# Kernel optimization log

Measured on AMD Instinct MI355X. Metric: run time of the kernel, lower is better.

## Reference

```python
import jax, jax.numpy as jnp
from jax import lax
import numpy as np

B, N, J, NI, D = 2, 2048, 24, 9, 3
CD, HID = 16, 128
SOFT_BLEND = 20.0
MAX_STEPS, CVG = 50, 1e-5
INIT_BONES = np.array([0, 1, 2, 4, 5, 16, 17, 18, 19])


def _mlp(params, x):
    h = x
    for W, b in params[:-1]:
        h = jax.nn.softplus(h @ W + b)
    W, b = params[-1]
    return h @ W + b


def _broyden(g, x0, J_inv0):
    # x0: [P,3,1], J_inv0: [P,3,3]; fixed MAX_STEPS iterations, track best iterate
    gx = g(x0)
    err0 = jnp.linalg.norm(gx, axis=(1, 2))
    state = (x0, gx, J_inv0, -(J_inv0 @ gx), x0, err0)

    def body(i, st):
        x, gx, Jinv, upd, bx, berr = st
        dx = upd
        x = x + dx
        gx_new = g(x)
        dgx = gx_new - gx
        vT = jnp.swapaxes(dx, -2, -1) @ Jinv            # [P,1,3]
        a = dx - Jinv @ dgx                              # [P,3,1]
        b = vT @ dgx + 1e-6                              # [P,1,1]
        Jinv = Jinv + (a / b) @ vT                       # rank-1 Broyden update
        upd = -(Jinv @ gx_new)
        err = jnp.linalg.norm(gx_new, axis=(1, 2))
        better = err < berr
        bx = jnp.where(better[:, None, None], x, bx)
        berr = jnp.where(better, err, berr)
        return (x, gx_new, Jinv, upd, bx, berr)

    st = lax.fori_loop(0, MAX_STEPS, body, state)
    return st[4], st[5] < CVG


def setup_inputs():
    key = jax.random.key(0)
    ks = jax.random.split(key, 24)
    xd = 0.5 * jax.random.normal(ks[0], (B, N, D), jnp.float32)
    cond_latent = jax.random.normal(ks[1], (B, CD), jnp.float32)
    # near-identity invertible bone transforms
    R = jnp.eye(3, dtype=jnp.float32) + 0.1 * jax.random.normal(ks[2], (B, J, 3, 3), jnp.float32)
    t = 0.1 * jax.random.normal(ks[3], (B, J, 3), jnp.float32)
    tfs = jnp.zeros((B, J, 4, 4), jnp.float32)
    tfs = tfs.at[..., :3, :3].set(R).at[..., :3, 3].set(t).at[..., 3, 3].set(1.0)

    def w(k, fi, fo):
        return jax.random.normal(k, (fi, fo), jnp.float32) / np.sqrt(fi)

    din = D + CD
    inp = dict(xd=xd, cond_latent=cond_latent, tfs=tfs)
    dims_lbs = [(din, HID), (HID, HID), (HID, HID), (HID, J)]
    dims_disp = [(din, HID), (HID, HID), (HID, HID), (HID, D)]
    for i, (fi, fo) in enumerate(dims_lbs):
        inp[f"lbs_w{i}"] = w(ks[4 + i], fi, fo)
        inp[f"lbs_b{i}"] = jnp.zeros((fo,), jnp.float32)
    for i, (fi, fo) in enumerate(dims_disp):
        inp[f"disp_w{i}"] = w(ks[10 + i], fi, fo)
        inp[f"disp_b{i}"] = jnp.zeros((fo,), jnp.float32)
    return inp


def _forward(xd, cond_latent, tfs, lbs, disp):
    P = B * N
    xd_f = xd.reshape(P, D)
    cond_f = jnp.broadcast_to(cond_latent[:, None], (B, N, CD)).reshape(P, CD)
    tfs_f = jnp.broadcast_to(tfs[:, None], (B, N, J, 4, 4)).reshape(P, J, 4, 4)

    # __init: inverse-skin xd with one-hot weights at each init bone -> [P, NI, 3]
    xd_h = jnp.concatenate([xd_f, jnp.ones((P, 1), xd.dtype)], -1)
    xc_init = jnp.einsum('pnij,pj->pni', jnp.linalg.inv(tfs_f[:, INIT_BONES]), xd_h)[..., :3]

    PI = P * NI
    cond_e = jnp.repeat(cond_f, NI, axis=0)       # [PI, CD]
    tfs_e = jnp.repeat(tfs_f, NI, axis=0)         # [PI, J, 4, 4]
    xd_tgt = jnp.repeat(xd_f, NI, axis=0)         # [PI, 3]
    x0 = xc_init.reshape(PI, D)

    def fwd_skin(xc, lbs_p, cond_p, tfs_p):
        w = jax.nn.softmax(SOFT_BLEND * _mlp(lbs_p, jnp.concatenate([xc, cond_p], -1)), -1)
        xh = jnp.concatenate([xc, jnp.ones_like(xc[:, :1])], -1)
        return jnp.einsum('pn,pnij,pj->pi', w, tfs_p, xh)[:, :3]

    def fwd_skin_pt(x, c, t, lbs_p):
        w = jax.nn.softmax(SOFT_BLEND * _mlp(lbs_p, jnp.concatenate([x, c])))
        xh = jnp.concatenate([x, jnp.ones((1,), x.dtype)])
        return jnp.einsum('n,nij,j->i', w, t, xh)[:3]

    def gradient(xc, lbs_p, cond_p, tfs_p):
        # per-point 3x3 Jacobian of forward skinning wrt canonical point
        f = lambda x, c, t: fwd_skin_pt(x, c, t, lbs_p)
        return jax.vmap(jax.jacfwd(f), in_axes=(0, 0, 0))(xc, cond_p, tfs_p)

    # stop-gradient copies for the no-grad broyden search (torch.no_grad block)
    sg = lax.stop_gradient
    lbs_sg = [(sg(W), sg(b)) for W, b in lbs]
    cond_sg, tfs_sg, xdt_sg = sg(cond_e), sg(tfs_e), sg(xd_tgt)

    J_inv0 = jnp.linalg.inv(gradient(sg(x0), lbs_sg, cond_sg, tfs_sg))

    def g_ng(x):  # x: [PI,3,1]
        return (fwd_skin(x[..., 0], lbs_sg, cond_sg, tfs_sg) - xdt_sg)[..., None]

    x_opt, valid = _broyden(g_ng, sg(x0)[..., None], J_inv0)
    xc_opt = sg(x_opt[..., 0])

    # implicit-differentiation correction (eval_mode=False path)
    xd_opt = fwd_skin(xc_opt, lbs, cond_e, tfs_e)
    grad_inv = jnp.linalg.inv(gradient(xc_opt, lbs, cond_e, tfs_e))
    corr = jnp.einsum('pij,pj->pi', -sg(grad_inv), xd_opt - sg(xd_opt))
    xc = xc_opt + corr

    # __query_cano: beta displacement network
    xc = xc + _mlp(disp, jnp.concatenate([xc, cond_e], -1))
    return xc.reshape(B, N, NI, D), valid.reshape(B, N, NI)


def reference(xd, cond_latent, tfs, lbs_w0, lbs_b0, lbs_w1, lbs_b1, lbs_w2, lbs_b2, lbs_w3, lbs_b3, disp_w0, disp_b0, disp_w1, disp_b1, disp_w2, disp_b2, disp_w3, disp_b3):
    lbs = [(lbs_w0, lbs_b0), (lbs_w1, lbs_b1), (lbs_w2, lbs_b2), (lbs_w3, lbs_b3)]
    disp = [(disp_w0, disp_b0), (disp_w1, disp_b1), (disp_w2, disp_b2), (disp_w3, disp_b3)]
    return _forward(xd, cond_latent, tfs, lbs, disp)
```

## Files before the change

### kernel.cpp

```cpp
#include <hip/hip_runtime.h>
#include <hip/hip_bf16.h>
#include <math.h>

#define NB 2
#define NN 2048
#define NJ 24
#define NIB 9
#define NCD 16
#define NHID 128
#define NP (NB * NN)
#define NPI (NP * NIB)
#define NBSTRIDE (NN * NIB)
#define SBLEND 20.0f
#define CVG_EPS 1e-5f
#define MAX_STEPS 50

#define HSTR 129
#define INSTRD 21
#define LSTR 25

static __device__ __forceinline__ float softplusf(float x) {
    return fmaxf(x, 0.0f) + log1pf(expf(-fabsf(x)));
}
static __device__ __forceinline__ float sigmoidf(float x) {
    return 1.0f / (1.0f + expf(-x));
}
static __device__ __forceinline__ int bone_of(int ib) {
    return (ib < 3) ? ib : ((ib < 5) ? ib + 1 : ib + 11);
}

template <int K>
static __device__ __forceinline__ void mv_acc32(const float* __restrict__ Wp, const float* inrow,
                                                int jb, float* acc) {
#pragma unroll 4
    for (int k = 0; k < K; k++) {
        float h = inrow[k];
        const float* wk = Wp + k * NHID + jb;
#pragma unroll
        for (int jj = 0; jj < 32; jj++) acc[jj] = fmaf(h, wk[jj], acc[jj]);
    }
}

template <int K, int LDIN>
static __device__ __forceinline__ void val_layer(const float* __restrict__ Wp,
                                                 const float* __restrict__ bp,
                                                 const float* inbase, float (*Hs)[HSTR], int r,
                                                 int jb, bool prebar) {
    float acc[32];
#pragma unroll
    for (int jj = 0; jj < 32; jj++) acc[jj] = bp[jb + jj];
    mv_acc32<K>(Wp, inbase + r * LDIN, jb, acc);
    if (prebar) __syncthreads();
#pragma unroll
    for (int jj = 0; jj < 32; jj++) Hs[r][jb + jj] = softplusf(acc[jj]);
    __syncthreads();
}

template <int K, int LDIN>
static __device__ __forceinline__ void jac_layer(const float* __restrict__ Wp,
                                                 const float* __restrict__ bp,
                                                 const float* inbase, float (*Hs)[HSTR], int r,
                                                 int jb, bool prebar) {
    const bool isval = (r < 16);
    const int p = r & 15;
    float acc[32];
#pragma unroll
    for (int jj = 0; jj < 32; jj++) acc[jj] = isval ? bp[jb + jj] : 0.0f;
    mv_acc32<K>(Wp, inbase + r * LDIN, jb, acc);
    if (prebar) __syncthreads();
#pragma unroll
    for (int jj = 0; jj < 32; jj++) Hs[r][jb + jj] = acc[jj];
    __syncthreads();
    float zv[32];
    if (!isval) {
#pragma unroll
        for (int jj = 0; jj < 32; jj++) zv[jj] = Hs[p][jb + jj];
    }
    __syncthreads();
    if (isval) {
#pragma unroll
        for (int jj = 0; jj < 32; jj++) Hs[r][jb + jj] = softplusf(acc[jj]);
    } else {
#pragma unroll
        for (int jj = 0; jj < 32; jj++) Hs[r][jb + jj] = sigmoidf(zv[jj]) * acc[jj];
    }
    __syncthreads();
}

template <int NC, int LDW, bool JAC>
static __device__ __forceinline__ void logit_layer(const float* __restrict__ Wp,
                                                   const float* __restrict__ bp,
                                                   const float* inbase, float (*Lgs)[LSTR], int r,
                                                   int wid) {
    const int jb = wid * NC;
    const bool isval = (!JAC) || (r < 16);
    float acc[NC];
#pragma unroll
    for (int jj = 0; jj < NC; jj++) acc[jj] = isval ? bp[jb + jj] : 0.0f;
#pragma unroll 4
    for (int k = 0; k < NHID; k++) {
        float h = inbase[r * HSTR + k];
        const float* wk = Wp + k * LDW + jb;
#pragma unroll
        for (int jj = 0; jj < NC; jj++) acc[jj] = fmaf(h, wk[jj], acc[jj]);
    }
#pragma unroll
    for (int jj = 0; jj < NC; jj++) Lgs[r][jb + jj] = acc[jj];
    __syncthreads();
}

__global__ __launch_bounds__(256) void kernel_fused(
    const float* __restrict__ xd, const float* __restrict__ cond, const float* __restrict__ tfs,
    const float* __restrict__ lw0, const float* __restrict__ lb0,
    const float* __restrict__ lw1, const float* __restrict__ lb1,
    const float* __restrict__ lw2, const float* __restrict__ lb2,
    const float* __restrict__ lw3, const float* __restrict__ lb3,
    const float* __restrict__ dw0, const float* __restrict__ db0,
    const float* __restrict__ dw1, const float* __restrict__ db1,
    const float* __restrict__ dw2, const float* __restrict__ db2,
    const float* __restrict__ dw3, const float* __restrict__ db3,
    float* __restrict__ out) {
    __shared__ float sIN[64][INSTRD];
    __shared__ float sH[64][HSTR];
    __shared__ float sLg[64][LSTR];
    __shared__ float sTm[NJ * 12];
    __shared__ int sFlag;

    const int tid = threadIdx.x;
    const int r = tid & 63;
    const int wid = __builtin_amdgcn_readfirstlane(tid >> 6);
    const int jb = wid * 32;
    const int pi0 = blockIdx.x * 64;
    const int b = pi0 / NBSTRIDE;
    const int pi = pi0 + r;

    for (int t = tid; t < NJ * 12; t += 256) {
        int j = t / 12, rc = t % 12;
        sTm[t] = tfs[(size_t)(b * NJ + j) * 16 + rc];
    }
    if (tid >= 16 && tid < 64) {
        const int d = (tid >> 4) - 1;
#pragma unroll
        for (int k = 0; k < 19; k++) sIN[tid][k] = (k == d) ? 1.0f : 0.0f;
    }
    if (tid < 16) {
#pragma unroll
        for (int cc = 0; cc < NCD; cc++) sIN[tid][3 + cc] = cond[b * NCD + cc];
    }

    float x0_ = 0, x1_ = 0, x2_ = 0, g0 = 0, g1 = 0, g2 = 0;
    float Ji0 = 0, Ji1 = 0, Ji2 = 0, Ji3 = 0, Ji4 = 0, Ji5 = 0, Ji6 = 0, Ji7 = 0, Ji8 = 0;
    float u0 = 0, u1 = 0, u2 = 0, bx0 = 0, bx1 = 0, bx2 = 0, berr = 0;
    float tx = 0, ty = 0, tz = 0;
    if (tid < 64) {
        const int pp = pi / NIB;
        tx = xd[pp * 3 + 0]; ty = xd[pp * 3 + 1]; tz = xd[pp * 3 + 2];
    }

#pragma unroll 1
    for (int pass = 0; pass < 4; ++pass) {
        __syncthreads();
        if ((tid >> 4) == pass) {
            const int p = tid & 15;
            const int ib = pi % NIB;
            const int bone = bone_of(ib);
            const float* T = tfs + (size_t)(b * NJ + bone) * 16;
            float r00 = T[0], r01 = T[1], r02 = T[2], t0 = T[3];
            float r10 = T[4], r11 = T[5], r12 = T[6], t1 = T[7];
            float r20 = T[8], r21 = T[9], r22 = T[10], t2 = T[11];
            float det = r00 * (r11 * r22 - r12 * r21) - r01 * (r10 * r22 - r12 * r20) +
                        r02 * (r10 * r21 - r11 * r20);
            float rd = 1.0f / det;
            float i00 = (r11 * r22 - r12 * r21) * rd, i01 = -(r01 * r22 - r02 * r21) * rd,
                  i02 = (r01 * r12 - r02 * r11) * rd;
            float i10 = -(r10 * r22 - r12 * r20) * rd, i11 = (r00 * r22 - r02 * r20) * rd,
                  i12 = -(r00 * r12 - r02 * r10) * rd;
            float i20 = (r10 * r21 - r11 * r20) * rd, i21 = -(r00 * r21 - r01 * r20) * rd,
                  i22 = (r00 * r11 - r01 * r10) * rd;
            float vx = tx - t0, vy = ty - t1, vz = tz - t2;
            x0_ = i00 * vx + i01 * vy + i02 * vz;
            x1_ = i10 * vx + i11 * vy + i12 * vz;
            x2_ = i20 * vx + i21 * vy + i22 * vz;
            sIN[p][0] = x0_; sIN[p][1] = x1_; sIN[p][2] = x2_;
        }
        __syncthreads();

        jac_layer<19, INSTRD>(lw0, lb0, &sIN[0][0], sH, r, jb, false);
        jac_layer<NHID, HSTR>(lw1, lb1, &sH[0][0], sH, r, jb, true);
        jac_layer<NHID, HSTR>(lw2, lb2, &sH[0][0], sH, r, jb, true);
        logit_layer<6, NJ, true>(lw3, lb3, &sH[0][0], sLg, r, wid);

        if ((tid >> 4) == pass) {
            const int p = tid & 15;
            float mx = -1e30f;
#pragma unroll
            for (int j = 0; j < NJ; j++) mx = fmaxf(mx, SBLEND * sLg[p][j]);
            float S = 0.0f;
#pragma unroll
            for (int j = 0; j < NJ; j++) S += expf(SBLEND * sLg[p][j] - mx);
            const float invS = 1.0f / S;
            float d0 = 0, d1 = 0, d2 = 0;
#pragma unroll
            for (int j = 0; j < NJ; j++) {
                float sj = expf(SBLEND * sLg[p][j] - mx) * invS;
                d0 += sj * (SBLEND * sLg[16 + p][j]);
                d1 += sj * (SBLEND * sLg[32 + p][j]);
                d2 += sj * (SBLEND * sLg[48 + p][j]);
            }
            float f0 = 0, f1 = 0, f2 = 0;
            float J00 = 0, J01 = 0, J02 = 0, J10 = 0, J11 = 0, J12 = 0, J20 = 0, J21 = 0,
                  J22 = 0;
#pragma unroll
            for (int j = 0; j < NJ; j++) {
                float sj = expf(SBLEND * sLg[p][j] - mx) * invS;
                float uj0 = SBLEND * sLg[16 + p][j], uj1 = SBLEND * sLg[32 + p][j],
                      uj2 = SBLEND * sLg[48 + p][j];
                float sd0 = sj * (uj0 - d0), sd1 = sj * (uj1 - d1), sd2 = sj * (uj2 - d2);
                const float* M = &sTm[j * 12];
                float y0 = M[0] * x0_ + M[1] * x1_ + M[2] * x2_ + M[3];
                float y1 = M[4] * x0_ + M[5] * x1_ + M[6] * x2_ + M[7];
                float y2 = M[8] * x0_ + M[9] * x1_ + M[10] * x2_ + M[11];
                f0 += sj * y0; f1 += sj * y1; f2 += sj * y2;
                J00 += sd0 * y0 + sj * M[0]; J01 += sd1 * y0 + sj * M[1]; J02 += sd2 * y0 + sj * M[2];
                J10 += sd0 * y1 + sj * M[4]; J11 += sd1 * y1 + sj * M[5]; J12 += sd2 * y1 + sj * M[6];
                J20 += sd0 * y2 + sj * M[8]; J21 += sd1 * y2 + sj * M[9]; J22 += sd2 * y2 + sj * M[10];
            }
            g0 = f0 - tx; g1 = f1 - ty; g2 = f2 - tz;
            float detJ = J00 * (J11 * J22 - J12 * J21) - J01 * (J10 * J22 - J12 * J20) +
                         J02 * (J10 * J21 - J11 * J20);
            float rdJ = 1.0f / detJ;
            Ji0 = (J11 * J22 - J12 * J21) * rdJ; Ji1 = -(J01 * J22 - J02 * J21) * rdJ;
            Ji2 = (J01 * J12 - J02 * J11) * rdJ;
            Ji3 = -(J10 * J22 - J12 * J20) * rdJ; Ji4 = (J00 * J22 - J02 * J20) * rdJ;
            Ji5 = -(J00 * J12 - J02 * J10) * rdJ;
            Ji6 = (J10 * J21 - J11 * J20) * rdJ; Ji7 = -(J00 * J21 - J01 * J20) * rdJ;
            Ji8 = (J00 * J11 - J01 * J10) * rdJ;
            u0 = -(Ji0 * g0 + Ji1 * g1 + Ji2 * g2);
            u1 = -(Ji3 * g0 + Ji4 * g1 + Ji5 * g2);
            u2 = -(Ji6 * g0 + Ji7 * g1 + Ji8 * g2);
            berr = sqrtf(g0 * g0 + g1 * g1 + g2 * g2);
            bx0 = x0_; bx1 = x1_; bx2 = x2_;
        }
    }

    if (tid < 64) {
#pragma unroll
        for (int cc = 0; cc < NCD; cc++) sIN[tid][3 + cc] = cond[b * NCD + cc];
    }

#pragma unroll 1
    for (int it = 0; it < MAX_STEPS; ++it) {
        float dx0 = 0, dx1 = 0, dx2 = 0;
        if (tid < 64) {
            dx0 = u0; dx1 = u1; dx2 = u2;
            x0_ += dx0; x1_ += dx1; x2_ += dx2;
            sIN[tid][0] = x0_; sIN[tid][1] = x1_; sIN[tid][2] = x2_;
        }
        __syncthreads();

        val_layer<19, INSTRD>(lw0, lb0, &sIN[0][0], sH, r, jb, false);
        val_layer<NHID, HSTR>(lw1, lb1, &sH[0][0], sH, r, jb, true);
        val_layer<NHID, HSTR>(lw2, lb2, &sH[0][0], sH, r, jb, true);
        logit_layer<6, NJ, false>(lw3, lb3, &sH[0][0], sLg, r, wid);

        if (tid < 64) {
            float mx = -1e30f;
#pragma unroll
            for (int j = 0; j < NJ; j++) mx = fmaxf(mx, SBLEND * sLg[r][j]);
            float S = 0.0f;
#pragma unroll
            for (int j = 0; j < NJ; j++) {
                float e = expf(SBLEND * sLg[r][j] - mx);
                sLg[r][j] = e;
                S += e;
            }
            const float invS = 1.0f / S;
            float f0 = 0, f1 = 0, f2 = 0;
#pragma unroll
            for (int j = 0; j < NJ; j++) {
                float sj = sLg[r][j] * invS;
                const float* M = &sTm[j * 12];
                f0 += sj * (M[0] * x0_ + M[1] * x1_ + M[2] * x2_ + M[3]);
                f1 += sj * (M[4] * x0_ + M[5] * x1_ + M[6] * x2_ + M[7]);
                f2 += sj * (M[8] * x0_ + M[9] * x1_ + M[10] * x2_ + M[11]);
            }
            float gn0 = f0 - tx, gn1 = f1 - ty, gn2 = f2 - tz;
            float dg0 = gn0 - g0, dg1 = gn1 - g1, dg2 = gn2 - g2;
            float Jd0 = Ji0 * dg0 + Ji1 * dg1 + Ji2 * dg2;
            float Jd1 = Ji3 * dg0 + Ji4 * dg1 + Ji5 * dg2;
            float Jd2 = Ji6 * dg0 + Ji7 * dg1 + Ji8 * dg2;
            float v0 = dx0 * Ji0 + dx1 * Ji3 + dx2 * Ji6;
            float v1 = dx0 * Ji1 + dx1 * Ji4 + dx2 * Ji7;
            float v2 = dx0 * Ji2 + dx1 * Ji5 + dx2 * Ji8;
            float a0 = dx0 - Jd0, a1 = dx1 - Jd1, a2 = dx2 - Jd2;
            float bden = v0 * dg0 + v1 * dg1 + v2 * dg2 + 1e-6f;
            float s0 = a0 / bden, s1 = a1 / bden, s2 = a2 / bden;
            Ji0 += s0 * v0; Ji1 += s0 * v1; Ji2 += s0 * v2;
            Ji3 += s1 * v0; Ji4 += s1 * v1; Ji5 += s1 * v2;
            Ji6 += s2 * v0; Ji7 += s2 * v1; Ji8 += s2 * v2;
            u0 = -(Ji0 * gn0 + Ji1 * gn1 + Ji2 * gn2);
            u1 = -(Ji3 * gn0 + Ji4 * gn1 + Ji5 * gn2);
            u2 = -(Ji6 * gn0 + Ji7 * gn1 + Ji8 * gn2);
            float err = sqrtf(gn0 * gn0 + gn1 * gn1 + gn2 * gn2);
            if (err < berr) { berr = err; bx0 = x0_; bx1 = x1_; bx2 = x2_; }
            g0 = gn0; g1 = gn1; g2 = gn2;
            int allc = __all(berr < CVG_EPS);
            if (tid == 0) sFlag = allc;
        }
        __syncthreads();
        if (sFlag) break;
    }

    if (tid < 64) {
        sIN[tid][0] = bx0; sIN[tid][1] = bx1; sIN[tid][2] = bx2;
    }
    __syncthreads();

    val_layer<19, INSTRD>(dw0, db0, &sIN[0][0], sH, r, jb, false);
    val_layer<NHID, HSTR>(dw1, db1, &sH[0][0], sH, r, jb, true);
    val_layer<NHID, HSTR>(dw2, db2, &sH[0][0], sH, r, jb, true);

    if (tid < 64) {
        float a0 = db3[0], a1 = db3[1], a2 = db3[2];
#pragma unroll 4
        for (int k = 0; k < NHID; k++) {
            float h = sH[tid][k];
            a0 = fmaf(h, dw3[k * 3 + 0], a0);
            a1 = fmaf(h, dw3[k * 3 + 1], a1);
            a2 = fmaf(h, dw3[k * 3 + 2], a2);
        }
        out[pi * 3 + 0] = bx0 + a0;
        out[pi * 3 + 1] = bx1 + a1;
        out[pi * 3 + 2] = bx2 + a2;
        out[3 * NPI + pi] = (berr < CVG_EPS) ? 1.0f : 0.0f;
    }
}

extern "C" void kernel_launch(void* const* d_in, const int* in_sizes, int n_in,
                              void* d_out, int out_size, void* d_ws, size_t ws_size,
                              hipStream_t stream) {
    (void)in_sizes; (void)n_in; (void)out_size; (void)d_ws; (void)ws_size;
    const float* xd   = (const float*)d_in[0];
    const float* cond = (const float*)d_in[1];
    const float* tfs  = (const float*)d_in[2];
    const float* lw0 = (const float*)d_in[3];  const float* lb0 = (const float*)d_in[4];
    const float* lw1 = (const float*)d_in[5];  const float* lb1 = (const float*)d_in[6];
    const float* lw2 = (const float*)d_in[7];  const float* lb2 = (const float*)d_in[8];
    const float* lw3 = (const float*)d_in[9];  const float* lb3 = (const float*)d_in[10];
    const float* dw0 = (const float*)d_in[11]; const float* db0 = (const float*)d_in[12];
    const float* dw1 = (const float*)d_in[13]; const float* db1 = (const float*)d_in[14];
    const float* dw2 = (const float*)d_in[15]; const float* db2 = (const float*)d_in[16];
    const float* dw3 = (const float*)d_in[17]; const float* db3 = (const float*)d_in[18];
    float* out = (float*)d_out;

    kernel_fused<<<NPI / 64, 256, 0, stream>>>(xd, cond, tfs, lw0, lb0, lw1, lb1, lw2, lb2,
                                               lw3, lb3, dw0, db0, dw1, db1, dw2, db2, dw3, db3,
                                               out);
}
```

Before: 1.499 ms.

## Restructure fused solver so each wavefront owns eight points without block barriers

```diff
diff --git a/kernel.cpp b/kernel.cpp
--- a/kernel.cpp
+++ b/kernel.cpp
@@ -1,5 +1,4 @@
 #include <hip/hip_runtime.h>
-#include <hip/hip_bf16.h>
 #include <math.h>
 
 #define NB 2
@@ -15,9 +14,10 @@
 #define CVG_EPS 1e-5f
 #define MAX_STEPS 50
 
+#define NTHR 256
+#define PPB 32
+#define NBLK (NPI / PPB)
 #define HSTR 129
-#define INSTRD 21
-#define LSTR 25
 
 static __device__ __forceinline__ float softplusf(float x) {
     return fmaxf(x, 0.0f) + log1pf(expf(-fabsf(x)));
@@ -29,87 +29,139 @@
     return (ib < 3) ? ib : ((ib < 5) ? ib + 1 : ib + 11);
 }
 
-template <int K>
-static __device__ __forceinline__ void mv_acc32(const float* __restrict__ Wp, const float* inrow,
-                                                int jb, float* acc) {
+template <int IMM>
+static __device__ __forceinline__ float swzf(float v) {
+    return __int_as_float(__builtin_amdgcn_ds_swizzle(__float_as_int(v), IMM));
+}
+
+static __device__ __forceinline__ void fma16q(float h, const float* __restrict__ wk,
+                                              float* acc) {
+    const float4 a = *(const float4*)(wk + 0);
+    const float4 b = *(const float4*)(wk + 4);
+    const float4 c = *(const float4*)(wk + 8);
+    const float4 d = *(const float4*)(wk + 12);
+    acc[0] = fmaf(h, a.x, acc[0]);   acc[1] = fmaf(h, a.y, acc[1]);
+    acc[2] = fmaf(h, a.z, acc[2]);   acc[3] = fmaf(h, a.w, acc[3]);
+    acc[4] = fmaf(h, b.x, acc[4]);   acc[5] = fmaf(h, b.y, acc[5]);
+    acc[6] = fmaf(h, b.z, acc[6]);   acc[7] = fmaf(h, b.w, acc[7]);
+    acc[8] = fmaf(h, c.x, acc[8]);   acc[9] = fmaf(h, c.y, acc[9]);
+    acc[10] = fmaf(h, c.z, acc[10]); acc[11] = fmaf(h, c.w, acc[11]);
+    acc[12] = fmaf(h, d.x, acc[12]); acc[13] = fmaf(h, d.y, acc[13]);
+    acc[14] = fmaf(h, d.z, acc[14]); acc[15] = fmaf(h, d.w, acc[15]);
+}
+static __device__ __forceinline__ void load16(const float* __restrict__ p, float* acc) {
+    const float4 a = *(const float4*)(p + 0);
+    const float4 b = *(const float4*)(p + 4);
+    const float4 c = *(const float4*)(p + 8);
+    const float4 d = *(const float4*)(p + 12);
+    acc[0] = a.x; acc[1] = a.y; acc[2] = a.z; acc[3] = a.w;
+    acc[4] = b.x; acc[5] = b.y; acc[6] = b.z; acc[7] = b.w;
+    acc[8] = c.x; acc[9] = c.y; acc[10] = c.z; acc[11] = c.w;
+    acc[12] = d.x; acc[13] = d.y; acc[14] = d.z; acc[15] = d.w;
+}
+
+static __device__ __forceinline__ void hid_val(const float* __restrict__ W,
+                                               const float* __restrict__ bias,
+                                               float* Hrow, int jb) {
+    float acc[16];
+    load16(bias + jb, acc);
 #pragma unroll 4
-    for (int k = 0; k < K; k++) {
-        float h = inrow[k];
-        const float* wk = Wp + k * NHID + jb;
-#pragma unroll
-        for (int jj = 0; jj < 32; jj++) acc[jj] = fmaf(h, wk[jj], acc[jj]);
-    }
-}
-
-template <int K, int LDIN>
-static __device__ __forceinline__ void val_layer(const float* __restrict__ Wp,
-                                                 const float* __restrict__ bp,
-                                                 const float* inbase, float (*Hs)[HSTR], int r,
-                                                 int jb, bool prebar) {
-    float acc[32];
-#pragma unroll
-    for (int jj = 0; jj < 32; jj++) acc[jj] = bp[jb + jj];
-    mv_acc32<K>(Wp, inbase + r * LDIN, jb, acc);
-    if (prebar) __syncthreads();
-#pragma unroll
-    for (int jj = 0; jj < 32; jj++) Hs[r][jb + jj] = softplusf(acc[jj]);
-    __syncthreads();
-}
-
-template <int K, int LDIN>
-static __device__ __forceinline__ void jac_layer(const float* __restrict__ Wp,
-                                                 const float* __restrict__ bp,
-                                                 const float* inbase, float (*Hs)[HSTR], int r,
-                                                 int jb, bool prebar) {
-    const bool isval = (r < 16);
-    const int p = r & 15;
-    float acc[32];
-#pragma unroll
-    for (int jj = 0; jj < 32; jj++) acc[jj] = isval ? bp[jb + jj] : 0.0f;
-    mv_acc32<K>(Wp, inbase + r * LDIN, jb, acc);
-    if (prebar) __syncthreads();
-#pragma unroll
-    for (int jj = 0; jj < 32; jj++) Hs[r][jb + jj] = acc[jj];
-    __syncthreads();
-    float zv[32];
-    if (!isval) {
-#pragma unroll
-        for (int jj = 0; jj < 32; jj++) zv[jj] = Hs[p][jb + jj];
-    }
-    __syncthreads();
+    for (int k = 0; k < NHID; k++) fma16q(Hrow[k], W + k * NHID + jb, acc);
+#pragma unroll
+    for (int jj = 0; jj < 16; jj++) Hrow[jb + jj] = softplusf(acc[jj]);
+}
+
+static __device__ __forceinline__ void hid_jac(const float* __restrict__ W,
+                                               const float* __restrict__ bias,
+                                               float* Hrow, float* Hval, int jb,
+                                               bool isval) {
+    float acc[16];
+    if (isval) load16(bias + jb, acc);
+    else {
+#pragma unroll
+        for (int jj = 0; jj < 16; jj++) acc[jj] = 0.0f;
+    }
+#pragma unroll 4
+    for (int k = 0; k < NHID; k++) fma16q(Hrow[k], W + k * NHID + jb, acc);
     if (isval) {
 #pragma unroll
-        for (int jj = 0; jj < 32; jj++) Hs[r][jb + jj] = softplusf(acc[jj]);
-    } else {
-#pragma unroll
-        for (int jj = 0; jj < 32; jj++) Hs[r][jb + jj] = sigmoidf(zv[jj]) * acc[jj];
-    }
-    __syncthreads();
-}
-
-template <int NC, int LDW, bool JAC>
-static __device__ __forceinline__ void logit_layer(const float* __restrict__ Wp,
-                                                   const float* __restrict__ bp,
-                                                   const float* inbase, float (*Lgs)[LSTR], int r,
-                                                   int wid) {
-    const int jb = wid * NC;
-    const bool isval = (!JAC) || (r < 16);
-    float acc[NC];
-#pragma unroll
-    for (int jj = 0; jj < NC; jj++) acc[jj] = isval ? bp[jb + jj] : 0.0f;
+        for (int jj = 0; jj < 16; jj++) Hrow[jb + jj] = acc[jj];
+    }
+#pragma unroll
+    for (int jj = 0; jj < 16; jj++) {
+        float zv = Hval[jb + jj];
+        Hrow[jb + jj] = isval ? softplusf(acc[jj]) : sigmoidf(zv) * acc[jj];
+    }
+}
+
+static __device__ __forceinline__ void logit_lay(const float* __restrict__ W,
+                                                 const float* __restrict__ bias,
+                                                 const float* Hrow, float* Lrow, int cg,
+                                                 bool addbias) {
+    const int jb3 = cg * 3;
+    float a0 = addbias ? bias[jb3 + 0] : 0.0f;
+    float a1 = addbias ? bias[jb3 + 1] : 0.0f;
+    float a2 = addbias ? bias[jb3 + 2] : 0.0f;
 #pragma unroll 4
     for (int k = 0; k < NHID; k++) {
-        float h = inbase[r * HSTR + k];
-        const float* wk = Wp + k * LDW + jb;
-#pragma unroll
-        for (int jj = 0; jj < NC; jj++) acc[jj] = fmaf(h, wk[jj], acc[jj]);
-    }
-#pragma unroll
-    for (int jj = 0; jj < NC; jj++) Lgs[r][jb + jj] = acc[jj];
-    __syncthreads();
-}
-
-__global__ __launch_bounds__(256) void kernel_fused(
+        float h = Hrow[k];
+        const float* w = W + k * NJ + jb3;
+        a0 = fmaf(h, w[0], a0); a1 = fmaf(h, w[1], a1); a2 = fmaf(h, w[2], a2);
+    }
+    Lrow[jb3 + 0] = a0; Lrow[jb3 + 1] = a1; Lrow[jb3 + 2] = a2;
+}
+
+static __device__ __forceinline__ void broyden_step(
+    float* sLgRow, const float* sTm, float tx, float ty, float tz,
+    float dx0, float dx1, float dx2,
+    float& x0_, float& x1_, float& x2_, float& g0, float& g1, float& g2,
+    float& Ji0, float& Ji1, float& Ji2, float& Ji3, float& Ji4, float& Ji5,
+    float& Ji6, float& Ji7, float& Ji8,
+    float& u0, float& u1, float& u2,
+    float& bx0, float& bx1, float& bx2, float& berr) {
+    float mx = -1e30f;
+#pragma unroll
+    for (int j = 0; j < NJ; j++) mx = fmaxf(mx, SBLEND * sLgRow[j]);
+    float S = 0.0f;
+#pragma unroll
+    for (int j = 0; j < NJ; j++) {
+        float e = expf(SBLEND * sLgRow[j] - mx);
+        sLgRow[j] = e;
+        S += e;
+    }
+    const float invS = 1.0f / S;
+    float f0 = 0, f1 = 0, f2 = 0;
+#pragma unroll
+    for (int j = 0; j < NJ; j++) {
+        float sj = sLgRow[j] * invS;
+        const float* M = &sTm[j * 12];
+        f0 += sj * (M[0] * x0_ + M[1] * x1_ + M[2] * x2_ + M[3]);
+        f1 += sj * (M[4] * x0_ + M[5] * x1_ + M[6] * x2_ + M[7]);
+        f2 += sj * (M[8] * x0_ + M[9] * x1_ + M[10] * x2_ + M[11]);
+    }
+    float gn0 = f0 - tx, gn1 = f1 - ty, gn2 = f2 - tz;
+    float dg0 = gn0 - g0, dg1 = gn1 - g1, dg2 = gn2 - g2;
+    float Jd0 = Ji0 * dg0 + Ji1 * dg1 + Ji2 * dg2;
+    float Jd1 = Ji3 * dg0 + Ji4 * dg1 + Ji5 * dg2;
+    float Jd2 = Ji6 * dg0 + Ji7 * dg1 + Ji8 * dg2;
+    float v0 = dx0 * Ji0 + dx1 * Ji3 + dx2 * Ji6;
+    float v1 = dx0 * Ji1 + dx1 * Ji4 + dx2 * Ji7;
+    float v2 = dx0 * Ji2 + dx1 * Ji5 + dx2 * Ji8;
+    float a0 = dx0 - Jd0, a1 = dx1 - Jd1, a2 = dx2 - Jd2;
+    float bden = v0 * dg0 + v1 * dg1 + v2 * dg2 + 1e-6f;
+    float s0 = a0 / bden, s1 = a1 / bden, s2 = a2 / bden;
+    Ji0 += s0 * v0; Ji1 += s0 * v1; Ji2 += s0 * v2;
+    Ji3 += s1 * v0; Ji4 += s1 * v1; Ji5 += s1 * v2;
+    Ji6 += s2 * v0; Ji7 += s2 * v1; Ji8 += s2 * v2;
+    u0 = -(Ji0 * gn0 + Ji1 * gn1 + Ji2 * gn2);
+    u1 = -(Ji3 * gn0 + Ji4 * gn1 + Ji5 * gn2);
+    u2 = -(Ji6 * gn0 + Ji7 * gn1 + Ji8 * gn2);
+    float err = sqrtf(gn0 * gn0 + gn1 * gn1 + gn2 * gn2);
+    if (err < berr) { berr = err; bx0 = x0_; bx1 = x1_; bx2 = x2_; }
+    g0 = gn0; g1 = gn1; g2 = gn2;
+}
+
+__global__ __launch_bounds__(NTHR) void kernel_fused(
     const float* __restrict__ xd, const float* __restrict__ cond, const float* __restrict__ tfs,
     const float* __restrict__ lw0, const float* __restrict__ lb0,
     const float* __restrict__ lw1, const float* __restrict__ lb1,
@@ -120,218 +172,202 @@
     const float* __restrict__ dw2, const float* __restrict__ db2,
     const float* __restrict__ dw3, const float* __restrict__ db3,
     float* __restrict__ out) {
-    __shared__ float sIN[64][INSTRD];
-    __shared__ float sH[64][HSTR];
-    __shared__ float sLg[64][LSTR];
+    __shared__ float sH[4][8][HSTR];
+    __shared__ float sLg[4][8][25];
     __shared__ float sTm[NJ * 12];
-    __shared__ int sFlag;
+    __shared__ float sCond[NCD];
 
     const int tid = threadIdx.x;
-    const int r = tid & 63;
+    const int lane = tid & 63;
     const int wid = __builtin_amdgcn_readfirstlane(tid >> 6);
-    const int jb = wid * 32;
-    const int pi0 = blockIdx.x * 64;
-    const int b = pi0 / NBSTRIDE;
-    const int pi = pi0 + r;
-
-    for (int t = tid; t < NJ * 12; t += 256) {
+    const int r = lane >> 3;
+    const int cg = lane & 7;
+    const int jb = cg * 16;
+    const int pi0w = blockIdx.x * PPB + wid * 8;
+    const int b = (blockIdx.x * PPB) / NBSTRIDE;
+    const int pi = pi0w + r;
+
+    for (int t = tid; t < NJ * 12; t += NTHR) {
         int j = t / 12, rc = t % 12;
         sTm[t] = tfs[(size_t)(b * NJ + j) * 16 + rc];
     }
-    if (tid >= 16 && tid < 64) {
-        const int d = (tid >> 4) - 1;
-#pragma unroll
-        for (int k = 0; k < 19; k++) sIN[tid][k] = (k == d) ? 1.0f : 0.0f;
-    }
-    if (tid < 16) {
-#pragma unroll
-        for (int cc = 0; cc < NCD; cc++) sIN[tid][3 + cc] = cond[b * NCD + cc];
-    }
+    if (tid < NCD) sCond[tid] = cond[b * NCD + tid];
+    __syncthreads();
+
+    float* Hw = &sH[wid][0][0];
+    float* Hrow = Hw + r * HSTR;
+    float* Hval = Hw + (r & 4) * HSTR;
+    float* Lw = &sLg[wid][0][0];
+    float* Lrow = Lw + r * 25;
+    const float* Lbase = Lw + (r & 4) * 25;
+
+    const int pp = pi / NIB;
+    const float tx = xd[pp * 3 + 0], ty = xd[pp * 3 + 1], tz = xd[pp * 3 + 2];
 
     float x0_ = 0, x1_ = 0, x2_ = 0, g0 = 0, g1 = 0, g2 = 0;
     float Ji0 = 0, Ji1 = 0, Ji2 = 0, Ji3 = 0, Ji4 = 0, Ji5 = 0, Ji6 = 0, Ji7 = 0, Ji8 = 0;
     float u0 = 0, u1 = 0, u2 = 0, bx0 = 0, bx1 = 0, bx2 = 0, berr = 0;
-    float tx = 0, ty = 0, tz = 0;
-    if (tid < 64) {
-        const int pp = pi / NIB;
-        tx = xd[pp * 3 + 0]; ty = xd[pp * 3 + 1]; tz = xd[pp * 3 + 2];
-    }
 
 #pragma unroll 1
-    for (int pass = 0; pass < 4; ++pass) {
-        __syncthreads();
-        if ((tid >> 4) == pass) {
-            const int p = tid & 15;
-            const int ib = pi % NIB;
-            const int bone = bone_of(ib);
-            const float* T = tfs + (size_t)(b * NJ + bone) * 16;
+    for (int p = 0; p < 4; ++p) {
+        const int q = pi0w + ((r < 4) ? p : p + 4);
+        const int ch = r & 3;
+        const bool isval = (ch == 0);
+        const int ppq = q / NIB;
+        const float txq = xd[ppq * 3 + 0], tyq = xd[ppq * 3 + 1], tzq = xd[ppq * 3 + 2];
+        float xq0, xq1, xq2;
+        {
+            const float* T = tfs + (size_t)(b * NJ + bone_of(q % NIB)) * 16;
             float r00 = T[0], r01 = T[1], r02 = T[2], t0 = T[3];
             float r10 = T[4], r11 = T[5], r12 = T[6], t1 = T[7];
             float r20 = T[8], r21 = T[9], r22 = T[10], t2 = T[11];
             float det = r00 * (r11 * r22 - r12 * r21) - r01 * (r10 * r22 - r12 * r20) +
                         r02 * (r10 * r21 - r11 * r20);
             float rd = 1.0f / det;
-            float i00 = (r11 * r22 - r12 * r21) * rd, i01 = -(r01 * r22 - r02 * r21) * rd,
-                  i02 = (r01 * r12 - r02 * r11) * rd;
-            float i10 = -(r10 * r22 - r12 * r20) * rd, i11 = (r00 * r22 - r02 * r20) * rd,
-                  i12 = -(r00 * r12 - r02 * r10) * rd;
-            float i20 = (r10 * r21 - r11 * r20) * rd, i21 = -(r00 * r21 - r01 * r20) * rd,
-                  i22 = (r00 * r11 - r01 * r10) * rd;
-            float vx = tx - t0, vy = ty - t1, vz = tz - t2;
-            x0_ = i00 * vx + i01 * vy + i02 * vz;
-            x1_ = i10 * vx + i11 * vy + i12 * vz;
-            x2_ = i20 * vx + i21 * vy + i22 * vz;
-            sIN[p][0] = x0_; sIN[p][1] = x1_; sIN[p][2] = x2_;
+            float vx = txq - t0, vy = tyq - t1, vz = tzq - t2;
+            xq0 = ((r11 * r22 - r12 * r21) * vx - (r01 * r22 - r02 * r21) * vy +
+                   (r01 * r12 - r02 * r11) * vz) * rd;
+            xq1 = (-(r10 * r22 - r12 * r20) * vx + (r00 * r22 - r02 * r20) * vy -
+                   (r00 * r12 - r02 * r10) * vz) * rd;
+            xq2 = ((r10 * r21 - r11 * r20) * vx - (r00 * r21 - r01 * r20) * vy +
+                   (r00 * r11 - r01 * r10) * vz) * rd;
         }
-        __syncthreads();
-
-        jac_layer<19, INSTRD>(lw0, lb0, &sIN[0][0], sH, r, jb, false);
-        jac_layer<NHID, HSTR>(lw1, lb1, &sH[0][0], sH, r, jb, true);
-        jac_layer<NHID, HSTR>(lw2, lb2, &sH[0][0], sH, r, jb, true);
-        logit_layer<6, NJ, true>(lw3, lb3, &sH[0][0], sLg, r, wid);
-
-        if ((tid >> 4) == pass) {
-            const int p = tid & 15;
+        {
+            float acc[16];
+            if (isval) {
+                load16(lb0 + jb, acc);
+                fma16q(xq0, lw0 + 0 * NHID + jb, acc);
+                fma16q(xq1, lw0 + 1 * NHID + jb, acc);
+                fma16q(xq2, lw0 + 2 * NHID + jb, acc);
+#pragma unroll
+                for (int k = 0; k < NCD; k++) fma16q(sCond[k], lw0 + (3 + k) * NHID + jb, acc);
+#pragma unroll
+                for (int jj = 0; jj < 16; jj++) Hrow[jb + jj] = acc[jj];
+            } else {
+                load16(lw0 + (ch - 1) * NHID + jb, acc);
+            }
+#pragma unroll
+            for (int jj = 0; jj < 16; jj++) {
+                float zv = Hval[jb + jj];
+                Hrow[jb + jj] = isval ? softplusf(acc[jj]) : sigmoidf(zv) * acc[jj];
+            }
+        }
+        hid_jac(lw1, lb1, Hrow, Hval, jb, isval);
+        hid_jac(lw2, lb2, Hrow, Hval, jb, isval);
+        logit_lay(lw3, lb3, Hrow, Lrow, cg, isval);
+
+        {
             float mx = -1e30f;
 #pragma unroll
-            for (int j = 0; j < NJ; j++) mx = fmaxf(mx, SBLEND * sLg[p][j]);
+            for (int j = 0; j < NJ; j++) mx = fmaxf(mx, SBLEND * Lbase[j]);
             float S = 0.0f;
 #pragma unroll
-            for (int j = 0; j < NJ; j++) S += expf(SBLEND * sLg[p][j] - mx);
+            for (int j = 0; j < NJ; j++) S += expf(SBLEND * Lbase[j] - mx);
             const float invS = 1.0f / S;
             float d0 = 0, d1 = 0, d2 = 0;
 #pragma unroll
             for (int j = 0; j < NJ; j++) {
-                float sj = expf(SBLEND * sLg[p][j] - mx) * invS;
-                d0 += sj * (SBLEND * sLg[16 + p][j]);
-                d1 += sj * (SBLEND * sLg[32 + p][j]);
-                d2 += sj * (SBLEND * sLg[48 + p][j]);
+                float sj = expf(SBLEND * Lbase[j] - mx) * invS;
+                d0 += sj * (SBLEND * Lbase[25 + j]);
+                d1 += sj * (SBLEND * Lbase[50 + j]);
+                d2 += sj * (SBLEND * Lbase[75 + j]);
             }
             float f0 = 0, f1 = 0, f2 = 0;
             float J00 = 0, J01 = 0, J02 = 0, J10 = 0, J11 = 0, J12 = 0, J20 = 0, J21 = 0,
                   J22 = 0;
 #pragma unroll
             for (int j = 0; j < NJ; j++) {
-                float sj = expf(SBLEND * sLg[p][j] - mx) * invS;
-                float uj0 = SBLEND * sLg[16 + p][j], uj1 = SBLEND * sLg[32 + p][j],
-                      uj2 = SBLEND * sLg[48 + p][j];
+                float sj = expf(SBLEND * Lbase[j] - mx) * invS;
+                float uj0 = SBLEND * Lbase[25 + j], uj1 = SBLEND * Lbase[50 + j],
+                      uj2 = SBLEND * Lbase[75 + j];
                 float sd0 = sj * (uj0 - d0), sd1 = sj * (uj1 - d1), sd2 = sj * (uj2 - d2);
                 const float* M = &sTm[j * 12];
-                float y0 = M[0] * x0_ + M[1] * x1_ + M[2] * x2_ + M[3];
-                float y1 = M[4] * x0_ + M[5] * x1_ + M[6] * x2_ + M[7];
-                float y2 = M[8] * x0_ + M[9] * x1_ + M[10] * x2_ + M[11];
+                float y0 = M[0] * xq0 + M[1] * xq1 + M[2] * xq2 + M[3];
+                float y1 = M[4] * xq0 + M[5] * xq1 + M[6] * xq2 + M[7];
+                float y2 = M[8] * xq0 + M[9] * xq1 + M[10] * xq2 + M[11];
                 f0 += sj * y0; f1 += sj * y1; f2 += sj * y2;
                 J00 += sd0 * y0 + sj * M[0]; J01 += sd1 * y0 + sj * M[1]; J02 += sd2 * y0 + sj * M[2];
                 J10 += sd0 * y1 + sj * M[4]; J11 += sd1 * y1 + sj * M[5]; J12 += sd2 * y1 + sj * M[6];
                 J20 += sd0 * y2 + sj * M[8]; J21 += sd1 * y2 + sj * M[9]; J22 += sd2 * y2 + sj * M[10];
             }
-            g0 = f0 - tx; g1 = f1 - ty; g2 = f2 - tz;
+            float gq0 = f0 - txq, gq1 = f1 - tyq, gq2 = f2 - tzq;
             float detJ = J00 * (J11 * J22 - J12 * J21) - J01 * (J10 * J22 - J12 * J20) +
                          J02 * (J10 * J21 - J11 * J20);
             float rdJ = 1.0f / detJ;
-            Ji0 = (J11 * J22 - J12 * J21) * rdJ; Ji1 = -(J01 * J22 - J02 * J21) * rdJ;
-            Ji2 = (J01 * J12 - J02 * J11) * rdJ;
-            Ji3 = -(J10 * J22 - J12 * J20) * rdJ; Ji4 = (J00 * J22 - J02 * J20) * rdJ;
-            Ji5 = -(J00 * J12 - J02 * J10) * rdJ;
-            Ji6 = (J10 * J21 - J11 * J20) * rdJ; Ji7 = -(J00 * J21 - J01 * J20) * rdJ;
-            Ji8 = (J00 * J11 - J01 * J10) * rdJ;
-            u0 = -(Ji0 * g0 + Ji1 * g1 + Ji2 * g2);
-            u1 = -(Ji3 * g0 + Ji4 * g1 + Ji5 * g2);
-            u2 = -(Ji6 * g0 + Ji7 * g1 + Ji8 * g2);
-            berr = sqrtf(g0 * g0 + g1 * g1 + g2 * g2);
-            bx0 = x0_; bx1 = x1_; bx2 = x2_;
+            float K0 = (J11 * J22 - J12 * J21) * rdJ, K1 = -(J01 * J22 - J02 * J21) * rdJ,
+                  K2 = (J01 * J12 - J02 * J11) * rdJ;
+            float K3 = -(J10 * J22 - J12 * J20) * rdJ, K4 = (J00 * J22 - J02 * J20) * rdJ,
+                  K5 = -(J00 * J12 - J02 * J10) * rdJ;
+            float K6 = (J10 * J21 - J11 * J20) * rdJ, K7 = -(J00 * J21 - J01 * J20) * rdJ,
+                  K8 = (J00 * J11 - J01 * J10) * rdJ;
+            if ((r & 3) == p) {
+                x0_ = xq0; x1_ = xq1; x2_ = xq2;
+                g0 = gq0; g1 = gq1; g2 = gq2;
+                Ji0 = K0; Ji1 = K1; Ji2 = K2; Ji3 = K3; Ji4 = K4; Ji5 = K5;
+                Ji6 = K6; Ji7 = K7; Ji8 = K8;
+                u0 = -(K0 * gq0 + K1 * gq1 + K2 * gq2);
+                u1 = -(K3 * gq0 + K4 * gq1 + K5 * gq2);
+                u2 = -(K6 * gq0 + K7 * gq1 + K8 * gq2);
+                berr = sqrtf(gq0 * gq0 + gq1 * gq1 + gq2 * gq2);
+                bx0 = xq0; bx1 = xq1; bx2 = xq2;
+            }
         }
-    }
-
-    if (tid < 64) {
-#pragma unroll
-        for (int cc = 0; cc < NCD; cc++) sIN[tid][3 + cc] = cond[b * NCD + cc];
     }
 
 #pragma unroll 1
     for (int it = 0; it < MAX_STEPS; ++it) {
-        float dx0 = 0, dx1 = 0, dx2 = 0;
-        if (tid < 64) {
-            dx0 = u0; dx1 = u1; dx2 = u2;
-            x0_ += dx0; x1_ += dx1; x2_ += dx2;
-            sIN[tid][0] = x0_; sIN[tid][1] = x1_; sIN[tid][2] = x2_;
+        float dx0 = u0, dx1 = u1, dx2 = u2;
+        x0_ += dx0; x1_ += dx1; x2_ += dx2;
+        {
+            float acc[16];
+            load16(lb0 + jb, acc);
+            fma16q(x0_, lw0 + 0 * NHID + jb, acc);
+            fma16q(x1_, lw0 + 1 * NHID + jb, acc);
+            fma16q(x2_, lw0 + 2 * NHID + jb, acc);
+#pragma unroll
+            for (int k = 0; k < NCD; k++) fma16q(sCond[k], lw0 + (3 + k) * NHID + jb, acc);
+#pragma unroll
+            for (int jj = 0; jj < 16; jj++) Hrow[jb + jj] = softplusf(acc[jj]);
         }
-        __syncthreads();
-
-        val_layer<19, INSTRD>(lw0, lb0, &sIN[0][0], sH, r, jb, false);
-        val_layer<NHID, HSTR>(lw1, lb1, &sH[0][0], sH, r, jb, true);
-        val_layer<NHID, HSTR>(lw2, lb2, &sH[0][0], sH, r, jb, true);
-        logit_layer<6, NJ, false>(lw3, lb3, &sH[0][0], sLg, r, wid);
-
-        if (tid < 64) {
-            float mx = -1e30f;
-#pragma unroll
-            for (int j = 0; j < NJ; j++) mx = fmaxf(mx, SBLEND * sLg[r][j]);
-            float S = 0.0f;
-#pragma unroll
-            for (int j = 0; j < NJ; j++) {
-                float e = expf(SBLEND * sLg[r][j] - mx);
-                sLg[r][j] = e;
-                S += e;
-            }
-            const float invS = 1.0f / S;
-            float f0 = 0, f1 = 0, f2 = 0;
-#pragma unroll
-            for (int j = 0; j < NJ; j++) {
-                float sj = sLg[r][j] * invS;
-                const float* M = &sTm[j * 12];
-                f0 += sj * (M[0] * x0_ + M[1] * x1_ + M[2] * x2_ + M[3]);
-                f1 += sj * (M[4] * x0_ + M[5] * x1_ + M[6] * x2_ + M[7]);
-                f2 += sj * (M[8] * x0_ + M[9] * x1_ + M[10] * x2_ + M[11]);
-            }
-            float gn0 = f0 - tx, gn1 = f1 - ty, gn2 = f2 - tz;
-            float dg0 = gn0 - g0, dg1 = gn1 - g1, dg2 = gn2 - g2;
-            float Jd0 = Ji0 * dg0 + Ji1 * dg1 + Ji2 * dg2;
-            float Jd1 = Ji3 * dg0 + Ji4 * dg1 + Ji5 * dg2;
-            float Jd2 = Ji6 * dg0 + Ji7 * dg1 + Ji8 * dg2;
-            float v0 = dx0 * Ji0 + dx1 * Ji3 + dx2 * Ji6;
-            float v1 = dx0 * Ji1 + dx1 * Ji4 + dx2 * Ji7;
-            float v2 = dx0 * Ji2 + dx1 * Ji5 + dx2 * Ji8;
-            float a0 = dx0 - Jd0, a1 = dx1 - Jd1, a2 = dx2 - Jd2;
-            float bden = v0 * dg0 + v1 * dg1 + v2 * dg2 + 1e-6f;
-            float s0 = a0 / bden, s1 = a1 / bden, s2 = a2 / bden;
-            Ji0 += s0 * v0; Ji1 += s0 * v1; Ji2 += s0 * v2;
-            Ji3 += s1 * v0; Ji4 += s1 * v1; Ji5 += s1 * v2;
-            Ji6 += s2 * v0; Ji7 += s2 * v1; Ji8 += s2 * v2;
-            u0 = -(Ji0 * gn0 + Ji1 * gn1 + Ji2 * gn2);
-            u1 = -(Ji3 * gn0 + Ji4 * gn1 + Ji5 * gn2);
-            u2 = -(Ji6 * gn0 + Ji7 * gn1 + Ji8 * gn2);
-            float err = sqrtf(gn0 * gn0 + gn1 * gn1 + gn2 * gn2);
-            if (err < berr) { berr = err; bx0 = x0_; bx1 = x1_; bx2 = x2_; }
-            g0 = gn0; g1 = gn1; g2 = gn2;
-            int allc = __all(berr < CVG_EPS);
-            if (tid == 0) sFlag = allc;
-        }
-        __syncthreads();
-        if (sFlag) break;
-    }
-
-    if (tid < 64) {
-        sIN[tid][0] = bx0; sIN[tid][1] = bx1; sIN[tid][2] = bx2;
-    }
-    __syncthreads();
-
-    val_layer<19, INSTRD>(dw0, db0, &sIN[0][0], sH, r, jb, false);
-    val_layer<NHID, HSTR>(dw1, db1, &sH[0][0], sH, r, jb, true);
-    val_layer<NHID, HSTR>(dw2, db2, &sH[0][0], sH, r, jb, true);
-
-    if (tid < 64) {
-        float a0 = db3[0], a1 = db3[1], a2 = db3[2];
-#pragma unroll 4
-        for (int k = 0; k < NHID; k++) {
-            float h = sH[tid][k];
-            a0 = fmaf(h, dw3[k * 3 + 0], a0);
-            a1 = fmaf(h, dw3[k * 3 + 1], a1);
-            a2 = fmaf(h, dw3[k * 3 + 2], a2);
-        }
-        out[pi * 3 + 0] = bx0 + a0;
-        out[pi * 3 + 1] = bx1 + a1;
-        out[pi * 3 + 2] = bx2 + a2;
+        hid_val(lw1, lb1, Hrow, jb);
+        hid_val(lw2, lb2, Hrow, jb);
+        logit_lay(lw3, lb3, Hrow, Lrow, cg, true);
+
+        broyden_step(Lrow, sTm, tx, ty, tz, dx0, dx1, dx2,
+                     x0_, x1_, x2_, g0, g1, g2,
+                     Ji0, Ji1, Ji2, Ji3, Ji4, Ji5, Ji6, Ji7, Ji8,
+                     u0, u1, u2, bx0, bx1, bx2, berr);
+        if (__all(berr < CVG_EPS)) break;
+    }
+
+    {
+        float acc[16];
+        load16(db0 + jb, acc);
+        fma16q(bx0, dw0 + 0 * NHID + jb, acc);
+        fma16q(bx1, dw0 + 1 * NHID + jb, acc);
+        fma16q(bx2, dw0 + 2 * NHID + jb, acc);
+#pragma unroll
+        for (int k = 0; k < NCD; k++) fma16q(sCond[k], dw0 + (3 + k) * NHID + jb, acc);
+#pragma unroll
+        for (int jj = 0; jj < 16; jj++) Hrow[jb + jj] = softplusf(acc[jj]);
+    }
+    hid_val(dw1, db1, Hrow, jb);
+    hid_val(dw2, db2, Hrow, jb);
+
+    float a0 = 0, a1 = 0, a2 = 0;
+#pragma unroll
+    for (int m = 0; m < 16; m++) {
+        float h = Hrow[jb + m];
+        const float* w = dw3 + (jb + m) * 3;
+        a0 = fmaf(h, w[0], a0); a1 = fmaf(h, w[1], a1); a2 = fmaf(h, w[2], a2);
+    }
+    a0 += swzf<0x041F>(a0); a0 += swzf<0x081F>(a0); a0 += swzf<0x101F>(a0);
+    a1 += swzf<0x041F>(a1); a1 += swzf<0x081F>(a1); a1 += swzf<0x101F>(a1);
+    a2 += swzf<0x041F>(a2); a2 += swzf<0x081F>(a2); a2 += swzf<0x101F>(a2);
+    if (cg == 0) {
+        out[pi * 3 + 0] = bx0 + a0 + db3[0];
+        out[pi * 3 + 1] = bx1 + a1 + db3[1];
+        out[pi * 3 + 2] = bx2 + a2 + db3[2];
         out[3 * NPI + pi] = (berr < CVG_EPS) ? 1.0f : 0.0f;
     }
 }
@@ -353,7 +389,7 @@
     const float* dw3 = (const float*)d_in[17]; const float* db3 = (const float*)d_in[18];
     float* out = (float*)d_out;
 
-    kernel_fused<<<NPI / 64, 256, 0, stream>>>(xd, cond, tfs, lw0, lb0, lw1, lb1, lw2, lb2,
-                                               lw3, lb3, dw0, db0, dw1, db1, dw2, db2, dw3, db3,
-                                               out);
-}
+    kernel_fused<<<NBLK, NTHR, 0, stream>>>(xd, cond, tfs, lw0, lb0, lw1, lb1, lw2, lb2,
+                                            lw3, lb3, dw0, db0, dw1, db1, dw2, db2, dw3,
+                                            db3, out);
+}
```

Measured after the change: 2.788 ms. 1.86x slower.
